# Optimization experiments

Measured on AMD Instinct MI355X. Metric: run time of the kernel, lower is better.

The kernel has to match this reference:

```python
import jax, jax.numpy as jnp
import numpy as np

IN_DIM = 2048
OUT_DIM = 2048
GRID_SIZE = 8
BATCH = 4096
LN_EPS = 1e-5


def setup_inputs() -> dict:
    key = jax.random.key(0)
    k_x, k_w = jax.random.split(key)
    x = jax.random.normal(k_x, (BATCH, IN_DIM), dtype=jnp.float32)
    spline_weight = jax.random.normal(k_w, (OUT_DIM, IN_DIM, GRID_SIZE), dtype=jnp.float32) * 0.1
    return {
        "x": x,
        "ln_weight": jnp.ones((IN_DIM,), jnp.float32),
        "ln_bias": jnp.zeros((IN_DIM,), jnp.float32),
        "spline_weight": spline_weight,
        "scale_base": jnp.ones((OUT_DIM, IN_DIM), jnp.float32),
        "bias": jnp.zeros((OUT_DIM,), jnp.float32),
        "rbf_beta": jnp.full((1,), 2.0, jnp.float32),
        "grid": jnp.linspace(-1.0, 1.0, GRID_SIZE, dtype=jnp.float32),
    }


def reference(x, ln_weight, ln_bias, spline_weight, scale_base, bias, rbf_beta, grid):
    # LayerNorm over last dim (eps=1e-5, elementwise affine)
    mu = jnp.mean(x, axis=-1, keepdims=True)
    var = jnp.mean(jnp.square(x - mu), axis=-1, keepdims=True)
    xn = (x - mu) * jax.lax.rsqrt(var + LN_EPS) * ln_weight + ln_bias  # (B, in)

    beta = jnp.clip(rbf_beta, 0.5, 6.0)  # (1,)
    # RBF basis: (B, in, G)
    basis = jnp.exp(-jnp.square(xn[..., None] - grid) * beta)

    # Torch einsum('bdig,oid->bod') broadcasts the singleton d of basis against
    # spline_weight's last axis and sums g; after .sum(-1) this equals
    # (sum_g basis) @ (sum_d spline_weight).T
    S = basis.sum(-1)              # (B, in)
    Wd = spline_weight.sum(-1)     # (out, in)
    spline_sum = jnp.einsum('bi,oi->bo', S, Wd)

    base_out = jnp.einsum('bi,oi->bo', xn, scale_base)
    return base_out + spline_sum + bias
```

## Files before the change

kernel.cpp:

```cpp
#include <hip/hip_runtime.h>
#include <hip/hip_bf16.h>
#include <stdint.h>

constexpr int IN_DIM   = 2048;
constexpr int OUT_DIM  = 2048;
constexpr int BATCH    = 4096;
constexpr int KDIM     = 2 * IN_DIM;
constexpr float LN_EPS = 1e-5f;

#define TILE 128
#define BK   64
constexpr int NK    = KDIM / BK;
constexpr int STAGE = TILE * BK;

typedef __attribute__((ext_vector_type(8))) short  short8;
typedef __attribute__((ext_vector_type(4))) float  f32x4;

__device__ __forceinline__ unsigned short f2bf(float f) {
  __hip_bfloat16 h = __float2bfloat16(f);
  return *reinterpret_cast<unsigned short*>(&h);
}
__device__ __forceinline__ unsigned pack2bf(float a, float b) {
  return (unsigned)f2bf(a) | ((unsigned)f2bf(b) << 16);
}

__global__ __launch_bounds__(256) void ln_rbf_kernel(
    const float* __restrict__ x, const float* __restrict__ lnw,
    const float* __restrict__ lnb, const float* __restrict__ betap,
    const float* __restrict__ grid, unsigned short* __restrict__ A)
{
  const int row = blockIdx.x;
  const int tid = threadIdx.x;
  const float4* xr = reinterpret_cast<const float4*>(x + (size_t)row * IN_DIM);
  float4 v0 = xr[tid];
  float4 v1 = xr[tid + 256];
  float s = (v0.x + v0.y) + (v0.z + v0.w) + (v1.x + v1.y) + (v1.z + v1.w);
  float q = v0.x * v0.x + v0.y * v0.y + v0.z * v0.z + v0.w * v0.w
          + v1.x * v1.x + v1.y * v1.y + v1.z * v1.z + v1.w * v1.w;
  #pragma unroll
  for (int off = 32; off > 0; off >>= 1) {
    s += __shfl_down(s, off, 64);
    q += __shfl_down(q, off, 64);
  }
  __shared__ float red[10];
  const int lane = tid & 63, wv = tid >> 6;
  if (lane == 0) { red[wv] = s; red[4 + wv] = q; }
  __syncthreads();
  if (tid == 0) {
    float ts = (red[0] + red[1]) + (red[2] + red[3]);
    float tq = (red[4] + red[5]) + (red[6] + red[7]);
    float mu  = ts * (1.0f / IN_DIM);
    float var = tq * (1.0f / IN_DIM) - mu * mu;
    red[8] = mu;
    red[9] = rsqrtf(var + LN_EPS);
  }
  __syncthreads();
  const float mu = red[8], rs = red[9];
  const float beta = fminf(fmaxf(betap[0], 0.5f), 6.0f);
  float g[8];
  #pragma unroll
  for (int i = 0; i < 8; i++) g[i] = grid[i];
  const float4* w4 = reinterpret_cast<const float4*>(lnw);
  const float4* b4 = reinterpret_cast<const float4*>(lnb);
  unsigned short* Ar = A + (size_t)row * KDIM;
  #pragma unroll
  for (int h = 0; h < 2; h++) {
    const int idx = tid + h * 256;
    float4 xv  = (h == 0) ? v0 : v1;
    float4 wv4 = w4[idx];
    float4 bv4 = b4[idx];
    float xa[4] = {xv.x, xv.y, xv.z, xv.w};
    float wa[4] = {wv4.x, wv4.y, wv4.z, wv4.w};
    float ba[4] = {bv4.x, bv4.y, bv4.z, bv4.w};
    float xn[4], S[4];
    #pragma unroll
    for (int c = 0; c < 4; c++) {
      float xnv = (xa[c] - mu) * rs * wa[c] + ba[c];
      xn[c] = xnv;
      float acc = 0.f;
      #pragma unroll
      for (int gg = 0; gg < 8; gg++) {
        float d = xnv - g[gg];
        acc += __expf(-beta * d * d);
      }
      S[c] = acc;
    }
    uint2 px, ps;
    px.x = pack2bf(xn[0], xn[1]);
    px.y = pack2bf(xn[2], xn[3]);
    ps.x = pack2bf(S[0], S[1]);
    ps.y = pack2bf(S[2], S[3]);
    *reinterpret_cast<uint2*>(Ar + idx * 4) = px;
    *reinterpret_cast<uint2*>(Ar + IN_DIM + idx * 4) = ps;
  }
}

constexpr int SW_F4   = OUT_DIM * IN_DIM * 2;
constexpr int SB_F4   = OUT_DIM * IN_DIM / 4;

__global__ __launch_bounds__(256) void pack_b_kernel(
    const float* __restrict__ sw, const float* __restrict__ sb,
    unsigned* __restrict__ Bu)
{
  const int g = blockIdx.x * 256 + threadIdx.x;
  const int lane = threadIdx.x & 63;
  if (g < SW_F4) {
    float4 v = reinterpret_cast<const float4*>(sw)[g];
    float s = (v.x + v.y) + (v.z + v.w);
    s += __shfl_xor(s, 1, 64);
    float hi = __shfl_down(s, 2, 64);
    if ((lane & 3) == 0) {
      const int i_lin = g >> 1;
      const int o = i_lin >> 11;
      const int i = i_lin & (IN_DIM - 1);
      Bu[(size_t)o * (KDIM / 2) + (IN_DIM / 2) + (i >> 1)] = pack2bf(s, hi);
    }
  } else {
    const int t = g - SW_F4;
    float4 v = reinterpret_cast<const float4*>(sb)[t];
    const int o  = t >> 9;
    const int i4 = t & 511;
    uint2 u;
    u.x = pack2bf(v.x, v.y);
    u.y = pack2bf(v.z, v.w);
    *reinterpret_cast<uint2*>(&Bu[(size_t)o * (KDIM / 2) + i4 * 2]) = u;
  }
}

__device__ __forceinline__ void gld_lds16(const unsigned short* g, unsigned short* l) {
  __builtin_amdgcn_global_load_lds(
      (const __attribute__((address_space(1))) void*)g,
      (__attribute__((address_space(3))) void*)l, 16, 0, 0);
}

__global__ __launch_bounds__(512) void gemm_kernel(
    const unsigned short* __restrict__ A, const unsigned short* __restrict__ Bm,
    const float* __restrict__ bias, float* __restrict__ out)
{
  __shared__ __align__(16) unsigned short As[2 * STAGE];
  __shared__ __align__(16) unsigned short Bs[2 * STAGE];
  __shared__ unsigned prod_done, cons_done;

  const int tid  = threadIdx.x;
  const int lane = tid & 63;
  const int wv   = tid >> 6;
  const int m0   = blockIdx.y * TILE;
  const int n0   = blockIdx.x * TILE;

  if (tid == 0) { prod_done = 0u; cons_done = 0u; }
  __syncthreads();

  if (wv >= 4) {
    const int p = wv - 4;
    const unsigned short* Ap[4];
    const unsigned short* Bp[4];
    unsigned short* lA[4];
    unsigned short* lB[4];
    #pragma unroll
    for (int j = 0; j < 4; j++) {
      const int seg  = j * 256 + p * 64 + lane;
      const int row  = seg >> 3;
      const int gcol = ((seg & 7) ^ (row & 7)) * 8;
      Ap[j] = A  + (size_t)(m0 + row) * KDIM + gcol;
      Bp[j] = Bm + (size_t)(n0 + row) * KDIM + gcol;
      lA[j] = &As[(j * 256 + p * 64) * 8];
      lB[j] = &Bs[(j * 256 + p * 64) * 8];
    }
    #pragma unroll 1
    for (int kt = 0; kt < NK; kt++) {
      if (kt >= 2) {
        const unsigned need = 4u * (unsigned)(kt - 1);
        while (__hip_atomic_load(&cons_done, __ATOMIC_ACQUIRE,
                                 __HIP_MEMORY_SCOPE_WORKGROUP) < need)
          __builtin_amdgcn_s_sleep(1);
      }
      const int slot = (kt & 1) * STAGE;
      const int koff = kt * BK;
      #pragma unroll
      for (int j = 0; j < 4; j++) gld_lds16(Ap[j] + koff, lA[j] + slot);
      #pragma unroll
      for (int j = 0; j < 4; j++) gld_lds16(Bp[j] + koff, lB[j] + slot);
      __builtin_amdgcn_s_waitcnt(0);
      if (lane == 0)
        __hip_atomic_fetch_add(&prod_done, 1u, __ATOMIC_RELEASE,
                               __HIP_MEMORY_SCOPE_WORKGROUP);
    }
    return;
  }

  const int wr   = wv >> 1;
  const int wc   = wv & 1;
  const int lrow = lane & 15;
  const int lkq  = lane >> 4;

  f32x4 acc[4][4] = {};

  #pragma unroll 1
  for (int kt = 0; kt < NK; kt++) {
    const unsigned need = 4u * (unsigned)(kt + 1);
    while (__hip_atomic_load(&prod_done, __ATOMIC_ACQUIRE,
                             __HIP_MEMORY_SCOPE_WORKGROUP) < need)
      __builtin_amdgcn_s_sleep(1);
    const int cur = (kt & 1) * STAGE;

    short8 af[2][4], bf[2][4];
    #pragma unroll
    for (int h = 0; h < 2; h++) {
      #pragma unroll
      for (int mi = 0; mi < 4; mi++) {
        const int r = wr * 64 + mi * 16 + lrow;
        af[h][mi] = *reinterpret_cast<const short8*>(
            &As[cur + r * BK + (((h << 2) | lkq) ^ (lrow & 7)) * 8]);
      }
      #pragma unroll
      for (int ni = 0; ni < 4; ni++) {
        const int r = wc * 64 + ni * 16 + lrow;
        bf[h][ni] = *reinterpret_cast<const short8*>(
            &Bs[cur + r * BK + (((h << 2) | lkq) ^ (lrow & 7)) * 8]);
      }
    }
    #pragma unroll
    for (int h = 0; h < 2; h++)
      #pragma unroll
      for (int mi = 0; mi < 4; mi++)
        #pragma unroll
        for (int ni = 0; ni < 4; ni++)
          acc[mi][ni] = __builtin_amdgcn_mfma_f32_16x16x32_bf16(
              af[h][mi], bf[h][ni], acc[mi][ni], 0, 0, 0);

    if (lane == 0)
      __hip_atomic_fetch_add(&cons_done, 1u, __ATOMIC_RELEASE,
                             __HIP_MEMORY_SCOPE_WORKGROUP);
  }

  const int rb = (lane >> 4) * 4;
  #pragma unroll
  for (int ni = 0; ni < 4; ni++) {
    const int col = n0 + wc * 64 + ni * 16 + lrow;
    const float bv = bias[col];
    #pragma unroll
    for (int mi = 0; mi < 4; mi++) {
      const int rowm = m0 + wr * 64 + mi * 16 + rb;
      #pragma unroll
      for (int r = 0; r < 4; r++)
        out[(size_t)(rowm + r) * OUT_DIM + col] = acc[mi][ni][r] + bv;
    }
  }
}

extern "C" void kernel_launch(void* const* d_in, const int* in_sizes, int n_in,
                              void* d_out, int out_size, void* d_ws, size_t ws_size,
                              hipStream_t stream) {
  const float* x    = (const float*)d_in[0];
  const float* lnw  = (const float*)d_in[1];
  const float* lnb  = (const float*)d_in[2];
  const float* sw   = (const float*)d_in[3];
  const float* sb   = (const float*)d_in[4];
  const float* bias = (const float*)d_in[5];
  const float* beta = (const float*)d_in[6];
  const float* grid = (const float*)d_in[7];
  float* out = (float*)d_out;

  unsigned short* A = (unsigned short*)d_ws;
  unsigned short* B = A + (size_t)BATCH * KDIM;

  hipLaunchKernelGGL(ln_rbf_kernel, dim3(BATCH), dim3(256), 0, stream,
                     x, lnw, lnb, beta, grid, A);
  hipLaunchKernelGGL(pack_b_kernel, dim3((SW_F4 + SB_F4) / 256), dim3(256), 0, stream,
                     sw, sb, (unsigned*)B);
  hipLaunchKernelGGL(gemm_kernel, dim3(OUT_DIM / TILE, BATCH / TILE), dim3(512), 0, stream,
                     A, B, bias, out);
}
```

Measured before the change: 312.1 us.

## Use three-slot BK=32 producer/consumer pipeline with deferred waitcnt and cached counters

Halves the K-step to 32 and moves from a double buffer to a triple buffer, with a new paired-row XOR swizzle in LDS. Producer waves keep one stage of loads in flight by waiting only on the previous stage's vmcnt before signalling it, and both sides cache the last counter value they read to skip repeated atomic polling. The aim is to hide more global-load latency behind the MFMA work. The cost is twice as many synchronisation rounds per tile and relaxed atomics on the producer side, which may weaken the ordering guarantees.

```diff
diff --git a/kernel.cpp b/kernel.cpp
--- a/kernel.cpp
+++ b/kernel.cpp
@@ -9,9 +9,10 @@
 constexpr float LN_EPS = 1e-5f;
 
 #define TILE 128
-#define BK   64
-constexpr int NK    = KDIM / BK;
-constexpr int STAGE = TILE * BK;
+#define BK   32
+constexpr int NK     = KDIM / BK;
+constexpr int SLOT   = TILE * BK;
+constexpr int NSLOT  = 3;
 
 typedef __attribute__((ext_vector_type(8))) short  short8;
 typedef __attribute__((ext_vector_type(4))) float  f32x4;
@@ -137,8 +138,8 @@
     const unsigned short* __restrict__ A, const unsigned short* __restrict__ Bm,
     const float* __restrict__ bias, float* __restrict__ out)
 {
-  __shared__ __align__(16) unsigned short As[2 * STAGE];
-  __shared__ __align__(16) unsigned short Bs[2 * STAGE];
+  __shared__ __align__(16) unsigned short As[NSLOT * SLOT];
+  __shared__ __align__(16) unsigned short Bs[NSLOT * SLOT];
   __shared__ unsigned prod_done, cons_done;
 
   const int tid  = threadIdx.x;
@@ -152,39 +153,49 @@
 
   if (wv >= 4) {
     const int p = wv - 4;
-    const unsigned short* Ap[4];
-    const unsigned short* Bp[4];
-    unsigned short* lA[4];
-    unsigned short* lB[4];
-    #pragma unroll
-    for (int j = 0; j < 4; j++) {
-      const int seg  = j * 256 + p * 64 + lane;
-      const int row  = seg >> 3;
-      const int gcol = ((seg & 7) ^ (row & 7)) * 8;
-      Ap[j] = A  + (size_t)(m0 + row) * KDIM + gcol;
-      Bp[j] = Bm + (size_t)(n0 + row) * KDIM + gcol;
-      lA[j] = &As[(j * 256 + p * 64) * 8];
-      lB[j] = &Bs[(j * 256 + p * 64) * 8];
-    }
+    const unsigned short* Ap[2];
+    const unsigned short* Bp[2];
+    unsigned aBase[2], bBase[2];
+    #pragma unroll
+    for (int j = 0; j < 2; j++) {
+      const int seg  = (p * 2 + j) * 64 + lane;
+      const int line = seg >> 3;
+      const int gi   = (seg & 7) ^ (line & 7);
+      const int row  = line * 2 + (gi >> 2);
+      const int kg   = gi & 3;
+      Ap[j] = A  + (size_t)(m0 + row) * KDIM + kg * 8;
+      Bp[j] = Bm + (size_t)(n0 + row) * KDIM + kg * 8;
+      aBase[j] = (unsigned)((p * 2 + j) * 512);
+      bBase[j] = aBase[j];
+    }
+    unsigned cdone = 0;
     #pragma unroll 1
     for (int kt = 0; kt < NK; kt++) {
-      if (kt >= 2) {
-        const unsigned need = 4u * (unsigned)(kt - 1);
-        while (__hip_atomic_load(&cons_done, __ATOMIC_ACQUIRE,
-                                 __HIP_MEMORY_SCOPE_WORKGROUP) < need)
-          __builtin_amdgcn_s_sleep(1);
-      }
-      const int slot = (kt & 1) * STAGE;
+      if (kt >= NSLOT) {
+        const unsigned need = 4u * (unsigned)(kt - NSLOT + 1);
+        while (cdone < need) {
+          cdone = __hip_atomic_load(&cons_done, __ATOMIC_RELAXED,
+                                    __HIP_MEMORY_SCOPE_WORKGROUP);
+          if (cdone < need) __builtin_amdgcn_s_sleep(1);
+        }
+      }
+      const unsigned slot = (unsigned)(kt % NSLOT) * SLOT;
       const int koff = kt * BK;
       #pragma unroll
-      for (int j = 0; j < 4; j++) gld_lds16(Ap[j] + koff, lA[j] + slot);
-      #pragma unroll
-      for (int j = 0; j < 4; j++) gld_lds16(Bp[j] + koff, lB[j] + slot);
-      __builtin_amdgcn_s_waitcnt(0);
-      if (lane == 0)
-        __hip_atomic_fetch_add(&prod_done, 1u, __ATOMIC_RELEASE,
-                               __HIP_MEMORY_SCOPE_WORKGROUP);
-    }
+      for (int j = 0; j < 2; j++) gld_lds16(Ap[j] + koff, &As[slot + aBase[j]]);
+      #pragma unroll
+      for (int j = 0; j < 2; j++) gld_lds16(Bp[j] + koff, &Bs[slot + bBase[j]]);
+      if (kt >= 1) {
+        __builtin_amdgcn_s_waitcnt(0x0F74);
+        if (lane == 0)
+          __hip_atomic_fetch_add(&prod_done, 1u, __ATOMIC_RELAXED,
+                                 __HIP_MEMORY_SCOPE_WORKGROUP);
+      }
+    }
+    __builtin_amdgcn_s_waitcnt(0x0F70);
+    if (lane == 0)
+      __hip_atomic_fetch_add(&prod_done, 1u, __ATOMIC_RELAXED,
+                             __HIP_MEMORY_SCOPE_WORKGROUP);
     return;
   }
 
@@ -193,54 +204,61 @@
   const int lrow = lane & 15;
   const int lkq  = lane >> 4;
 
+  unsigned aOff[4], bOff[4];
+  #pragma unroll
+  for (int i = 0; i < 4; i++) {
+    const int ra = wr * 64 + i * 16 + lrow;
+    const int la = ra >> 1, ga = (ra & 1) * 4 + lkq;
+    aOff[i] = (unsigned)(la * 64 + (ga ^ (la & 7)) * 8);
+    const int rb = wc * 64 + i * 16 + lrow;
+    const int lb = rb >> 1, gb = (rb & 1) * 4 + lkq;
+    bOff[i] = (unsigned)(lb * 64 + (gb ^ (lb & 7)) * 8);
+  }
+
   f32x4 acc[4][4] = {};
+  unsigned ready = 0;
 
   #pragma unroll 1
   for (int kt = 0; kt < NK; kt++) {
     const unsigned need = 4u * (unsigned)(kt + 1);
-    while (__hip_atomic_load(&prod_done, __ATOMIC_ACQUIRE,
-                             __HIP_MEMORY_SCOPE_WORKGROUP) < need)
-      __builtin_amdgcn_s_sleep(1);
-    const int cur = (kt & 1) * STAGE;
-
-    short8 af[2][4], bf[2][4];
-    #pragma unroll
-    for (int h = 0; h < 2; h++) {
-      #pragma unroll
-      for (int mi = 0; mi < 4; mi++) {
-        const int r = wr * 64 + mi * 16 + lrow;
-        af[h][mi] = *reinterpret_cast<const short8*>(
-            &As[cur + r * BK + (((h << 2) | lkq) ^ (lrow & 7)) * 8]);
-      }
-      #pragma unroll
-      for (int ni = 0; ni < 4; ni++) {
-        const int r = wc * 64 + ni * 16 + lrow;
-        bf[h][ni] = *reinterpret_cast<const short8*>(
-            &Bs[cur + r * BK + (((h << 2) | lkq) ^ (lrow & 7)) * 8]);
-      }
-    }
-    #pragma unroll
-    for (int h = 0; h < 2; h++)
-      #pragma unroll
-      for (int mi = 0; mi < 4; mi++)
-        #pragma unroll
-        for (int ni = 0; ni < 4; ni++)
-          acc[mi][ni] = __builtin_amdgcn_mfma_f32_16x16x32_bf16(
-              af[h][mi], bf[h][ni], acc[mi][ni], 0, 0, 0);
+    if (ready < need) {
+      while (true) {
+        ready = __hip_atomic_load(&prod_done, __ATOMIC_ACQUIRE,
+                                  __HIP_MEMORY_SCOPE_WORKGROUP);
+        if (ready >= need) break;
+        __builtin_amdgcn_s_sleep(1);
+      }
+    }
+    const unsigned cur = (unsigned)(kt % NSLOT) * SLOT;
+
+    short8 af[4], bf[4];
+    #pragma unroll
+    for (int mi = 0; mi < 4; mi++)
+      af[mi] = *reinterpret_cast<const short8*>(&As[cur + aOff[mi]]);
+    #pragma unroll
+    for (int ni = 0; ni < 4; ni++)
+      bf[ni] = *reinterpret_cast<const short8*>(&Bs[cur + bOff[ni]]);
+
+    #pragma unroll
+    for (int mi = 0; mi < 4; mi++)
+      #pragma unroll
+      for (int ni = 0; ni < 4; ni++)
+        acc[mi][ni] = __builtin_amdgcn_mfma_f32_16x16x32_bf16(
+            af[mi], bf[ni], acc[mi][ni], 0, 0, 0);
 
     if (lane == 0)
       __hip_atomic_fetch_add(&cons_done, 1u, __ATOMIC_RELEASE,
                              __HIP_MEMORY_SCOPE_WORKGROUP);
   }
 
-  const int rb = (lane >> 4) * 4;
+  const int rbse = (lane >> 4) * 4;
   #pragma unroll
   for (int ni = 0; ni < 4; ni++) {
     const int col = n0 + wc * 64 + ni * 16 + lrow;
     const float bv = bias[col];
     #pragma unroll
     for (int mi = 0; mi < 4; mi++) {
-      const int rowm = m0 + wr * 64 + mi * 16 + rb;
+      const int rowm = m0 + wr * 64 + mi * 16 + rbse;
       #pragma unroll
       for (int r = 0; r < 4; r++)
         out[(size_t)(rowm + r) * OUT_DIM + col] = acc[mi][ni][r] + bv;
```

After: 323.9 us. 3.8% more time.
